# Optimization experiments

Measured on AMD Instinct MI355X. Metric: run time of the kernel, lower is better.

The kernel has to match this reference:

```python
import jax, jax.numpy as jnp
import numpy as np

VOCAB = 32000
EMB = 32
HID = 64
B = 1024
T = 512


def setup_inputs() -> dict:
    key = jax.random.key(0)
    ks = jax.random.split(key, 8)
    s_e = 1.0 / np.sqrt(EMB)
    s_h = 1.0 / np.sqrt(HID)
    return {
        "x": jax.random.randint(ks[0], (B, T), 0, VOCAB),
        "emb": jax.random.normal(ks[1], (VOCAB, EMB), jnp.float32),
        "W_ih": jax.random.uniform(ks[2], (4 * HID, EMB), jnp.float32, -s_h, s_h),
        "W_hh": jax.random.uniform(ks[3], (4 * HID, HID), jnp.float32, -s_h, s_h),
        "b_ih": jax.random.uniform(ks[4], (4 * HID,), jnp.float32, -s_h, s_h),
        "b_hh": jax.random.uniform(ks[5], (4 * HID,), jnp.float32, -s_h, s_h),
        "fc_W": jax.random.uniform(ks[6], (VOCAB, HID), jnp.float32, -s_h, s_h),
        "fc_b": jax.random.uniform(ks[7], (VOCAB,), jnp.float32, -s_h, s_h),
    }


def reference(x, emb, W_ih, W_hh, b_ih, b_hh, fc_W, fc_b):
    e = emb[x]  # [B, T, EMB]
    # Precompute input contribution to all gates for all timesteps: [B, T, 4H]
    xg = jnp.einsum("bte,ge->btg", e, W_ih) + b_ih + b_hh
    xg_t = jnp.transpose(xg, (1, 0, 2))  # [T, B, 4H] for scan over time

    def step(carry, xg_step):
        h, c = carry
        gates = xg_step + h @ W_hh.T  # [B, 4H]
        i, f, g, o = jnp.split(gates, 4, axis=-1)  # torch gate order i,f,g,o
        i = jax.nn.sigmoid(i)
        f = jax.nn.sigmoid(f)
        g = jnp.tanh(g)
        o = jax.nn.sigmoid(o)
        c = f * c + i * g
        h = o * jnp.tanh(c)
        return (h, c), None

    h0 = jnp.zeros((x.shape[0], HID), e.dtype)
    c0 = jnp.zeros((x.shape[0], HID), e.dtype)
    (h_last, _), _ = jax.lax.scan(step, (h0, c0), xg_t)
    # out[:, -1, :] of the LSTM is just the final hidden state
    return h_last @ fc_W.T + fc_b  # [B, VOCAB]
```

## Files before the change

### kernel.cpp

```cpp
#include <hip/hip_runtime.h>
#include <cstddef>
#include <cstdint>

#define VOCAB 32000
#define EMB 32
#define HID 64
#define NG 256
#define BATCH 1024
#define SEQ 512
#define NB 4
#define ROWB 72
#define PFD 8
#define SEQP (SEQ + PFD)

#define L2E 1.44269504088896340736f

typedef short short8 __attribute__((ext_vector_type(8)));
typedef _Float16 half8 __attribute__((ext_vector_type(8)));
typedef float floatx4 __attribute__((ext_vector_type(4)));
typedef int int4v __attribute__((ext_vector_type(4)));

union FragH {
  half8 h;
  int4v v;
};

#define K1_ROWS 32
__global__ __launch_bounds__(256) void build_table(
    const float* __restrict__ emb, const float* __restrict__ W_ih,
    const float* __restrict__ b_ih, const float* __restrict__ b_hh,
    float* __restrict__ table) {
  __shared__ __align__(16) float erow[K1_ROWS * EMB];
  const int tid = threadIdx.x;
  const int v0 = blockIdx.x * K1_ROWS;
  const int gidx = (tid & 3) * 64 + (tid >> 2);
  const float sc = ((tid & 3) == 2) ? (2.0f * L2E) : (-L2E);

  float w[EMB];
#pragma unroll
  for (int e = 0; e < EMB; e += 4) {
    const float4 t = *(const float4*)&W_ih[gidx * EMB + e];
    w[e] = t.x; w[e + 1] = t.y; w[e + 2] = t.z; w[e + 3] = t.w;
  }
  const float bsum = b_ih[gidx] + b_hh[gidx];

  ((float4*)erow)[tid] = ((const float4*)&emb[(size_t)v0 * EMB])[tid];
  __syncthreads();

#pragma unroll 4
  for (int r = 0; r < K1_ROWS; ++r) {
    float acc = bsum;
#pragma unroll
    for (int e = 0; e < EMB; ++e) acc += erow[r * EMB + e] * w[e];
    table[(size_t)(v0 + r) * NG + tid] = acc * sc;
  }
}

__global__ __launch_bounds__(256, 1) void lstm_mfma(
    const int* __restrict__ x, const float* __restrict__ table,
    const float* __restrict__ W_hh, float* __restrict__ h_out) {
  __shared__ __align__(16) _Float16 Hs[2][16 * ROWB];
  __shared__ int xls[NB * SEQP];

  const int tid = threadIdx.x;
  const int w = tid >> 6;
  const int lane = tid & 63;
  const int quad = lane >> 4;
  const int col = lane & 15;
  const int blk = blockIdx.x;
  const int myhid = w * 16 + col;

  {
    int* hz = (int*)&Hs[0][0];
    const int nz = (int)(sizeof(Hs) / 4);
    for (int i = tid; i < nz; i += 256) hz[i] = 0;
  }
  {
    const int* xsrc = &x[(size_t)blk * NB * SEQ];
    for (int i = tid; i < NB * SEQ; i += 256) {
      const int q = i >> 9;
      const int t = i & (SEQ - 1);
      xls[q * SEQP + t] = xsrc[i] << 10;
    }
    if (tid < NB * PFD) {
      const int q = tid >> 3;
      const int t = tid & (PFD - 1);
      xls[q * SEQP + SEQ + t] = xsrc[q * SEQ + SEQ - 1] << 10;
    }
  }

  FragH Bf[4][2];
#pragma unroll
  for (int ti = 0; ti < 4; ++ti) {
    const int n = (w + ti * 4) * 16 + col;
    const float sc = (ti == 2) ? (2.0f * L2E) : (-L2E);
#pragma unroll
    for (int ko = 0; ko < 2; ++ko) {
      const float* src = &W_hh[n * HID + ko * 32 + quad * 8];
#pragma unroll
      for (int j = 0; j < 8; ++j) Bf[ti][ko].h[j] = (_Float16)(src[j] * sc);
    }
  }

  const floatx4 z4 = (floatx4){0.f, 0.f, 0.f, 0.f};

  float cs = 0.0f, hcur = 0.0f;

  __syncthreads();

  const int xrow = quad * SEQP;
  const char* __restrict__ tb4 = (const char*)(table + (size_t)myhid * 4);

  auto gather = [&](int tt) -> floatx4 {
    return *(const floatx4*)(tb4 + xls[xrow + tt]);
  };

  floatx4 xg0 = gather(0), xg1 = gather(1), xg2 = gather(2), xg3 = gather(3);
  floatx4 xg4 = gather(4), xg5 = gather(5), xg6 = gather(6), xg7 = gather(7);

  auto step = [&](floatx4& XG, const int RB, const int TT) {
    const float xi = XG[0], xf = XG[1], xgg = XG[2], xo = XG[3];
    XG = gather(TT + PFD);

    const int abase = col * ROWB + quad * 8;
    FragH A0, A1;
    A0.v = *(const int4v*)&Hs[RB][abase];
    A1.v = *(const int4v*)&Hs[RB][abase + 32];

    float pre0, pre1, pre2, pre3;
    {
      floatx4 r00 = __builtin_amdgcn_mfma_f32_16x16x32_f16(A0.h, Bf[0][0].h, z4, 0, 0, 0);
      floatx4 r01 = __builtin_amdgcn_mfma_f32_16x16x32_f16(A1.h, Bf[0][1].h, z4, 0, 0, 0);
      floatx4 r10 = __builtin_amdgcn_mfma_f32_16x16x32_f16(A0.h, Bf[1][0].h, z4, 0, 0, 0);
      floatx4 r11 = __builtin_amdgcn_mfma_f32_16x16x32_f16(A1.h, Bf[1][1].h, z4, 0, 0, 0);
      floatx4 r20 = __builtin_amdgcn_mfma_f32_16x16x32_f16(A0.h, Bf[2][0].h, z4, 0, 0, 0);
      floatx4 r21 = __builtin_amdgcn_mfma_f32_16x16x32_f16(A1.h, Bf[2][1].h, z4, 0, 0, 0);
      floatx4 r30 = __builtin_amdgcn_mfma_f32_16x16x32_f16(A0.h, Bf[3][0].h, z4, 0, 0, 0);
      floatx4 r31 = __builtin_amdgcn_mfma_f32_16x16x32_f16(A1.h, Bf[3][1].h, z4, 0, 0, 0);
      pre0 = (r00[0] + r01[0]) + xi;
      pre1 = (r10[0] + r11[0]) + xf;
      pre2 = (r20[0] + r21[0]) + xgg;
      pre3 = (r30[0] + r31[0]) + xo;
    }

    {
      const float gi = __builtin_amdgcn_rcpf(1.0f + __builtin_amdgcn_exp2f(pre0));
      const float gf = __builtin_amdgcn_rcpf(1.0f + __builtin_amdgcn_exp2f(pre1));
      const float rg = __builtin_amdgcn_rcpf(1.0f + __builtin_amdgcn_exp2f(pre2));
      const float go = __builtin_amdgcn_rcpf(1.0f + __builtin_amdgcn_exp2f(pre3));
      const float gg2 = fmaf(-4.0f * L2E, rg, 2.0f * L2E);
      cs = fmaf(gi, gg2, gf * cs);
      const float rc = __builtin_amdgcn_rcpf(1.0f + __builtin_amdgcn_exp2f(cs));
      hcur = go * fmaf(-2.0f, rc, 1.0f);
      Hs[RB ^ 1][(quad * 4) * ROWB + myhid] = (_Float16)hcur;
    }
    asm volatile("s_waitcnt lgkmcnt(0)\n\ts_barrier" ::: "memory");
  };

  for (int t = 0; t < SEQ; t += 8) {
    step(xg0, 0, t);
    step(xg1, 1, t + 1);
    step(xg2, 0, t + 2);
    step(xg3, 1, t + 3);
    step(xg4, 0, t + 4);
    step(xg5, 1, t + 5);
    step(xg6, 0, t + 6);
    step(xg7, 1, t + 7);
  }

  h_out[((size_t)blk * NB + quad) * HID + myhid] = hcur;
}

#define FC_BB 128
#define FC_BV 128
#define FC_PAD 4
__global__ __launch_bounds__(256) void fc_kernel(
    const float* __restrict__ h, const float* __restrict__ fc_W,
    const float* __restrict__ fc_b, float* __restrict__ out) {
  __shared__ __align__(16) float sh[HID][FC_BB + FC_PAD];
  __shared__ __align__(16) float sw[HID][FC_BV + FC_PAD];
  const int tid = threadIdx.x;
  const int v0 = blockIdx.x * FC_BV;
  const int b0 = blockIdx.y * FC_BB;
  const int ti = tid >> 4;
  const int tj = tid & 15;

  const float4 bias0 = *(const float4*)&fc_b[v0 + tj * 4];
  const float4 bias1 = *(const float4*)&fc_b[v0 + 64 + tj * 4];

  {
    const float4* src = (const float4*)&h[(size_t)b0 * HID];
#pragma unroll
    for (int i = 0; i < 8; ++i) {
      const int idx = tid + i * 256;
      const float4 t = src[idx];
      const int bl = idx >> 4;
      const int k = (idx * 4) & (HID - 1);
      sh[k][bl] = t.x; sh[k + 1][bl] = t.y; sh[k + 2][bl] = t.z; sh[k + 3][bl] = t.w;
    }
    const float4* wsrc = (const float4*)&fc_W[(size_t)v0 * HID];
#pragma unroll
    for (int i = 0; i < 8; ++i) {
      const int idx = tid + i * 256;
      const float4 t = wsrc[idx];
      const int vl = idx >> 4;
      const int k = (idx * 4) & (HID - 1);
      sw[k][vl] = t.x; sw[k + 1][vl] = t.y; sw[k + 2][vl] = t.z; sw[k + 3][vl] = t.w;
    }
  }
  __syncthreads();

  float acc[8][8];
#pragma unroll
  for (int i = 0; i < 8; ++i)
#pragma unroll
    for (int j = 0; j < 8; ++j) acc[i][j] = 0.0f;

#pragma unroll 4
  for (int k = 0; k < HID; ++k) {
    const float4 h0 = *(const float4*)&sh[k][ti * 8];
    const float4 h1 = *(const float4*)&sh[k][ti * 8 + 4];
    const float4 w0 = *(const float4*)&sw[k][tj * 4];
    const float4 w1 = *(const float4*)&sw[k][64 + tj * 4];
    const float hv[8] = {h0.x, h0.y, h0.z, h0.w, h1.x, h1.y, h1.z, h1.w};
    const float wv[8] = {w0.x, w0.y, w0.z, w0.w, w1.x, w1.y, w1.z, w1.w};
#pragma unroll
    for (int i = 0; i < 8; ++i)
#pragma unroll
      for (int j = 0; j < 8; ++j) acc[i][j] += hv[i] * wv[j];
  }

#pragma unroll
  for (int i = 0; i < 8; ++i) {
    const size_t row = (size_t)(b0 + ti * 8 + i) * VOCAB;
    floatx4 o0, o1;
    o0[0] = acc[i][0] + bias0.x; o0[1] = acc[i][1] + bias0.y;
    o0[2] = acc[i][2] + bias0.z; o0[3] = acc[i][3] + bias0.w;
    o1[0] = acc[i][4] + bias1.x; o1[1] = acc[i][5] + bias1.y;
    o1[2] = acc[i][6] + bias1.z; o1[3] = acc[i][7] + bias1.w;
    __builtin_nontemporal_store(o0, (floatx4*)&out[row + v0 + tj * 4]);
    __builtin_nontemporal_store(o1, (floatx4*)&out[row + v0 + 64 + tj * 4]);
  }
}

extern "C" void kernel_launch(void* const* d_in, const int* in_sizes, int n_in,
                              void* d_out, int out_size, void* d_ws, size_t ws_size,
                              hipStream_t stream) {
  const int* x = (const int*)d_in[0];
  const float* emb = (const float*)d_in[1];
  const float* W_ih = (const float*)d_in[2];
  const float* W_hh = (const float*)d_in[3];
  const float* b_ih = (const float*)d_in[4];
  const float* b_hh = (const float*)d_in[5];
  const float* fc_W = (const float*)d_in[6];
  const float* fc_b = (const float*)d_in[7];
  float* out = (float*)d_out;

  float* table = out;
  float* hbuf = (float*)d_ws;

  build_table<<<VOCAB / K1_ROWS, 256, 0, stream>>>(emb, W_ih, b_ih, b_hh, table);
  lstm_mfma<<<BATCH / NB, 256, 0, stream>>>(x, table, W_hh, hbuf);
  dim3 g3(VOCAB / FC_BV, BATCH / FC_BB);
  fc_kernel<<<g3, 256, 0, stream>>>(hbuf, fc_W, fc_b, out);
}
```

Before: 348.8 us.

## Port final FC to split-fp16 MFMA and fold input gates into LSTM accumulators

Replaces the FP32 scalar-FMA output projection with an MFMA kernel. Each wave keeps a 32-column slice of fc_W in registers as hi/lo fp16 pairs and streams batch rows, using three-term split-precision products to approximate fp32 accuracy. It also seeds the LSTM step's MFMA accumulators with the precomputed input-gate values and chains the two K-halves, removing the separate adds. The FC rewrite trades the shared-memory tiled GEMM for 250 blocks of narrow 4-byte scattered nontemporal stores, which may hurt write efficiency. Grid occupancy also drops.

Result: slower. 377.2 us (+8.1%).

```diff
diff --git a/kernel.cpp b/kernel.cpp
--- a/kernel.cpp
+++ b/kernel.cpp
@@ -119,7 +119,8 @@
   floatx4 xg4 = gather(4), xg5 = gather(5), xg6 = gather(6), xg7 = gather(7);
 
   auto step = [&](floatx4& XG, const int RB, const int TT) {
-    const float xi = XG[0], xf = XG[1], xgg = XG[2], xo = XG[3];
+    floatx4 c0 = z4, c1 = z4, c2 = z4, c3 = z4;
+    c0[0] = XG[0]; c1[0] = XG[1]; c2[0] = XG[2]; c3[0] = XG[3];
     XG = gather(TT + PFD);
 
     const int abase = col * ROWB + quad * 8;
@@ -127,27 +128,20 @@
     A0.v = *(const int4v*)&Hs[RB][abase];
     A1.v = *(const int4v*)&Hs[RB][abase + 32];
 
-    float pre0, pre1, pre2, pre3;
+    floatx4 r0 = __builtin_amdgcn_mfma_f32_16x16x32_f16(A0.h, Bf[0][0].h, c0, 0, 0, 0);
+    r0 = __builtin_amdgcn_mfma_f32_16x16x32_f16(A1.h, Bf[0][1].h, r0, 0, 0, 0);
+    floatx4 r1 = __builtin_amdgcn_mfma_f32_16x16x32_f16(A0.h, Bf[1][0].h, c1, 0, 0, 0);
+    r1 = __builtin_amdgcn_mfma_f32_16x16x32_f16(A1.h, Bf[1][1].h, r1, 0, 0, 0);
+    floatx4 r2 = __builtin_amdgcn_mfma_f32_16x16x32_f16(A0.h, Bf[2][0].h, c2, 0, 0, 0);
+    r2 = __builtin_amdgcn_mfma_f32_16x16x32_f16(A1.h, Bf[2][1].h, r2, 0, 0, 0);
+    floatx4 r3 = __builtin_amdgcn_mfma_f32_16x16x32_f16(A0.h, Bf[3][0].h, c3, 0, 0, 0);
+    r3 = __builtin_amdgcn_mfma_f32_16x16x32_f16(A1.h, Bf[3][1].h, r3, 0, 0, 0);
+
     {
-      floatx4 r00 = __builtin_amdgcn_mfma_f32_16x16x32_f16(A0.h, Bf[0][0].h, z4, 0, 0, 0);
-      floatx4 r01 = __builtin_amdgcn_mfma_f32_16x16x32_f16(A1.h, Bf[0][1].h, z4, 0, 0, 0);
-      floatx4 r10 = __builtin_amdgcn_mfma_f32_16x16x32_f16(A0.h, Bf[1][0].h, z4, 0, 0, 0);
-      floatx4 r11 = __builtin_amdgcn_mfma_f32_16x16x32_f16(A1.h, Bf[1][1].h, z4, 0, 0, 0);
-      floatx4 r20 = __builtin_amdgcn_mfma_f32_16x16x32_f16(A0.h, Bf[2][0].h, z4, 0, 0, 0);
-      floatx4 r21 = __builtin_amdgcn_mfma_f32_16x16x32_f16(A1.h, Bf[2][1].h, z4, 0, 0, 0);
-      floatx4 r30 = __builtin_amdgcn_mfma_f32_16x16x32_f16(A0.h, Bf[3][0].h, z4, 0, 0, 0);
-      floatx4 r31 = __builtin_amdgcn_mfma_f32_16x16x32_f16(A1.h, Bf[3][1].h, z4, 0, 0, 0);
-      pre0 = (r00[0] + r01[0]) + xi;
-      pre1 = (r10[0] + r11[0]) + xf;
-      pre2 = (r20[0] + r21[0]) + xgg;
-      pre3 = (r30[0] + r31[0]) + xo;
-    }
-
-    {
-      const float gi = __builtin_amdgcn_rcpf(1.0f + __builtin_amdgcn_exp2f(pre0));
-      const float gf = __builtin_amdgcn_rcpf(1.0f + __builtin_amdgcn_exp2f(pre1));
-      const float rg = __builtin_amdgcn_rcpf(1.0f + __builtin_amdgcn_exp2f(pre2));
-      const float go = __builtin_amdgcn_rcpf(1.0f + __builtin_amdgcn_exp2f(pre3));
+      const float gi = __builtin_amdgcn_rcpf(1.0f + __builtin_amdgcn_exp2f(r0[0]));
+      const float gf = __builtin_amdgcn_rcpf(1.0f + __builtin_amdgcn_exp2f(r1[0]));
+      const float rg = __builtin_amdgcn_rcpf(1.0f + __builtin_amdgcn_exp2f(r2[0]));
+      const float go = __builtin_amdgcn_rcpf(1.0f + __builtin_amdgcn_exp2f(r3[0]));
       const float gg2 = fmaf(-4.0f * L2E, rg, 2.0f * L2E);
       cs = fmaf(gi, gg2, gf * cs);
       const float rc = __builtin_amdgcn_rcpf(1.0f + __builtin_amdgcn_exp2f(cs));
@@ -171,75 +165,86 @@
   h_out[((size_t)blk * NB + quad) * HID + myhid] = hcur;
 }
 
-#define FC_BB 128
-#define FC_BV 128
-#define FC_PAD 4
-__global__ __launch_bounds__(256) void fc_kernel(
+#define FCV 128
+__global__ __launch_bounds__(256, 1) void fc_mfma(
     const float* __restrict__ h, const float* __restrict__ fc_W,
     const float* __restrict__ fc_b, float* __restrict__ out) {
-  __shared__ __align__(16) float sh[HID][FC_BB + FC_PAD];
-  __shared__ __align__(16) float sw[HID][FC_BV + FC_PAD];
   const int tid = threadIdx.x;
-  const int v0 = blockIdx.x * FC_BV;
-  const int b0 = blockIdx.y * FC_BB;
-  const int ti = tid >> 4;
-  const int tj = tid & 15;
-
-  const float4 bias0 = *(const float4*)&fc_b[v0 + tj * 4];
-  const float4 bias1 = *(const float4*)&fc_b[v0 + 64 + tj * 4];
-
-  {
-    const float4* src = (const float4*)&h[(size_t)b0 * HID];
-#pragma unroll
-    for (int i = 0; i < 8; ++i) {
-      const int idx = tid + i * 256;
-      const float4 t = src[idx];
-      const int bl = idx >> 4;
-      const int k = (idx * 4) & (HID - 1);
-      sh[k][bl] = t.x; sh[k + 1][bl] = t.y; sh[k + 2][bl] = t.z; sh[k + 3][bl] = t.w;
-    }
-    const float4* wsrc = (const float4*)&fc_W[(size_t)v0 * HID];
-#pragma unroll
-    for (int i = 0; i < 8; ++i) {
-      const int idx = tid + i * 256;
-      const float4 t = wsrc[idx];
-      const int vl = idx >> 4;
-      const int k = (idx * 4) & (HID - 1);
-      sw[k][vl] = t.x; sw[k + 1][vl] = t.y; sw[k + 2][vl] = t.z; sw[k + 3][vl] = t.w;
-    }
-  }
-  __syncthreads();
-
-  float acc[8][8];
-#pragma unroll
-  for (int i = 0; i < 8; ++i)
-#pragma unroll
-    for (int j = 0; j < 8; ++j) acc[i][j] = 0.0f;
-
-#pragma unroll 4
-  for (int k = 0; k < HID; ++k) {
-    const float4 h0 = *(const float4*)&sh[k][ti * 8];
-    const float4 h1 = *(const float4*)&sh[k][ti * 8 + 4];
-    const float4 w0 = *(const float4*)&sw[k][tj * 4];
-    const float4 w1 = *(const float4*)&sw[k][64 + tj * 4];
-    const float hv[8] = {h0.x, h0.y, h0.z, h0.w, h1.x, h1.y, h1.z, h1.w};
-    const float wv[8] = {w0.x, w0.y, w0.z, w0.w, w1.x, w1.y, w1.z, w1.w};
-#pragma unroll
-    for (int i = 0; i < 8; ++i)
-#pragma unroll
-      for (int j = 0; j < 8; ++j) acc[i][j] += hv[i] * wv[j];
-  }
-
-#pragma unroll
-  for (int i = 0; i < 8; ++i) {
-    const size_t row = (size_t)(b0 + ti * 8 + i) * VOCAB;
-    floatx4 o0, o1;
-    o0[0] = acc[i][0] + bias0.x; o0[1] = acc[i][1] + bias0.y;
-    o0[2] = acc[i][2] + bias0.z; o0[3] = acc[i][3] + bias0.w;
-    o1[0] = acc[i][4] + bias1.x; o1[1] = acc[i][5] + bias1.y;
-    o1[2] = acc[i][6] + bias1.z; o1[3] = acc[i][7] + bias1.w;
-    __builtin_nontemporal_store(o0, (floatx4*)&out[row + v0 + tj * 4]);
-    __builtin_nontemporal_store(o1, (floatx4*)&out[row + v0 + 64 + tj * 4]);
+  const int w = tid >> 6;
+  const int lane = tid & 63;
+  const int q = lane >> 4;
+  const int c = lane & 15;
+  const int nbase = blockIdx.x * FCV + w * 32;
+
+  const floatx4 z4 = (floatx4){0.f, 0.f, 0.f, 0.f};
+
+  FragH Bh[2][2], Bl[2][2];
+#pragma unroll
+  for (int nt = 0; nt < 2; ++nt) {
+#pragma unroll
+    for (int ko = 0; ko < 2; ++ko) {
+      const float* src = &fc_W[(size_t)(nbase + nt * 16 + c) * HID + ko * 32 + q * 8];
+#pragma unroll
+      for (int j = 0; j < 8; ++j) {
+        const float f = src[j];
+        const _Float16 hi = (_Float16)f;
+        Bh[nt][ko].h[j] = hi;
+        Bl[nt][ko].h[j] = (_Float16)(f - (float)hi);
+      }
+    }
+  }
+  const float bias0 = fc_b[nbase + c];
+  const float bias1 = fc_b[nbase + 16 + c];
+
+  auto loadh = [&](int mc, floatx4& a0, floatx4& a1, floatx4& a2, floatx4& a3) {
+    const float* hr = &h[(size_t)(mc * 16 + c) * HID + q * 8];
+    a0 = *(const floatx4*)hr;
+    a1 = *(const floatx4*)(hr + 4);
+    a2 = *(const floatx4*)(hr + 32);
+    a3 = *(const floatx4*)(hr + 36);
+  };
+
+  floatx4 p0, p1, p2, p3, n0, n1, n2, n3;
+  loadh(0, p0, p1, p2, p3);
+
+  for (int mc = 0; mc < BATCH / 16; ++mc) {
+    if (mc + 1 < BATCH / 16) loadh(mc + 1, n0, n1, n2, n3);
+
+    FragH Ah0, Al0, Ah1, Al1;
+#pragma unroll
+    for (int j = 0; j < 4; ++j) {
+      float f = p0[j];
+      _Float16 hi = (_Float16)f;
+      Ah0.h[j] = hi; Al0.h[j] = (_Float16)(f - (float)hi);
+      f = p1[j]; hi = (_Float16)f;
+      Ah0.h[4 + j] = hi; Al0.h[4 + j] = (_Float16)(f - (float)hi);
+      f = p2[j]; hi = (_Float16)f;
+      Ah1.h[j] = hi; Al1.h[j] = (_Float16)(f - (float)hi);
+      f = p3[j]; hi = (_Float16)f;
+      Ah1.h[4 + j] = hi; Al1.h[4 + j] = (_Float16)(f - (float)hi);
+    }
+
+    floatx4 acc0 = __builtin_amdgcn_mfma_f32_16x16x32_f16(Ah0.h, Bh[0][0].h, z4, 0, 0, 0);
+    floatx4 acc1 = __builtin_amdgcn_mfma_f32_16x16x32_f16(Ah0.h, Bh[1][0].h, z4, 0, 0, 0);
+    acc0 = __builtin_amdgcn_mfma_f32_16x16x32_f16(Ah1.h, Bh[0][1].h, acc0, 0, 0, 0);
+    acc1 = __builtin_amdgcn_mfma_f32_16x16x32_f16(Ah1.h, Bh[1][1].h, acc1, 0, 0, 0);
+    acc0 = __builtin_amdgcn_mfma_f32_16x16x32_f16(Al0.h, Bh[0][0].h, acc0, 0, 0, 0);
+    acc1 = __builtin_amdgcn_mfma_f32_16x16x32_f16(Al0.h, Bh[1][0].h, acc1, 0, 0, 0);
+    acc0 = __builtin_amdgcn_mfma_f32_16x16x32_f16(Al1.h, Bh[0][1].h, acc0, 0, 0, 0);
+    acc1 = __builtin_amdgcn_mfma_f32_16x16x32_f16(Al1.h, Bh[1][1].h, acc1, 0, 0, 0);
+    acc0 = __builtin_amdgcn_mfma_f32_16x16x32_f16(Ah0.h, Bl[0][0].h, acc0, 0, 0, 0);
+    acc1 = __builtin_amdgcn_mfma_f32_16x16x32_f16(Ah0.h, Bl[1][0].h, acc1, 0, 0, 0);
+    acc0 = __builtin_amdgcn_mfma_f32_16x16x32_f16(Ah1.h, Bl[0][1].h, acc0, 0, 0, 0);
+    acc1 = __builtin_amdgcn_mfma_f32_16x16x32_f16(Ah1.h, Bl[1][1].h, acc1, 0, 0, 0);
+
+#pragma unroll
+    for (int r = 0; r < 4; ++r) {
+      const size_t row = (size_t)(mc * 16 + q * 4 + r) * VOCAB;
+      __builtin_nontemporal_store(acc0[r] + bias0, &out[row + nbase + c]);
+      __builtin_nontemporal_store(acc1[r] + bias1, &out[row + nbase + 16 + c]);
+    }
+
+    p0 = n0; p1 = n1; p2 = n2; p3 = n3;
   }
 }
 
@@ -261,6 +266,5 @@
 
   build_table<<<VOCAB / K1_ROWS, 256, 0, stream>>>(emb, W_ih, b_ih, b_hh, table);
   lstm_mfma<<<BATCH / NB, 256, 0, stream>>>(x, table, W_hh, hbuf);
-  dim3 g3(VOCAB / FC_BV, BATCH / FC_BB);
-  fc_kernel<<<g3, 256, 0, stream>>>(hbuf, fc_W, fc_b, out);
-}
+  fc_mfma<<<VOCAB / FCV, 256, 0, stream>>>(hbuf, fc_W, fc_b, out);
+}
```
